# Optimization experiments

Measured on AMD Instinct MI355X. Metric: run time of the kernel, lower is better.

Reference implementation:

```python
import jax, jax.numpy as jnp
import numpy as np

B, D, H = 16384, 64, 128
L = D - 1  # number of per-dimension sub-networks (layers 1..dim-1)
W_SCALE = 0.05  # keep alpha outputs small so exp(alpha) stays well-conditioned


def setup_inputs() -> dict:
    key = jax.random.key(0)
    ks = jax.random.split(key, 8)
    return {
        "x": jax.random.normal(ks[0], (B, D), dtype=jnp.float32),
        "W1": jax.random.normal(ks[1], (L, D - 1, H), dtype=jnp.float32) * W_SCALE,
        "b1": jax.random.normal(ks[2], (L, H), dtype=jnp.float32) * W_SCALE,
        "W2": jax.random.normal(ks[3], (L, H, H), dtype=jnp.float32) * W_SCALE,
        "b2": jax.random.normal(ks[4], (L, H), dtype=jnp.float32) * W_SCALE,
        "W3": jax.random.normal(ks[5], (L, H, 2), dtype=jnp.float32) * W_SCALE,
        "b3": jax.random.normal(ks[6], (L, 2), dtype=jnp.float32) * W_SCALE,
        "initial_param": jax.random.uniform(
            ks[7], (2,), dtype=jnp.float32,
            minval=-np.sqrt(0.5), maxval=np.sqrt(0.5)),
    }


def reference(x, W1, b1, W2, b2, W3, b3, initial_param):
    # x: [B, D]. Layer l (l=0..L-1) corresponds to dim i=l+1 and consumes
    # x[:, :l+1]; we realize the ragged inputs via a triangular mask on W1.
    b, d = x.shape
    # mask[l, j] = 1 if input feature j is visible to layer l (j <= l)
    mask = (jnp.arange(d - 1)[None, :] <= jnp.arange(L)[:, None]).astype(x.dtype)
    W1m = W1 * mask[:, :, None]                       # [L, D-1, H]
    h = jnp.tanh(jnp.einsum('bd,ldh->blh', x[:, :d - 1], W1m) + b1)  # [B, L, H]
    h = jnp.tanh(jnp.einsum('blh,lhk->blk', h, W2) + b2)             # [B, L, H]
    out = jnp.einsum('blh,lho->blo', h, W3) + b3                     # [B, L, 2]
    mu0 = jnp.broadcast_to(initial_param[0], (b, 1))
    a0 = jnp.broadcast_to(initial_param[1], (b, 1))
    mu = jnp.concatenate([mu0, out[..., 0]], axis=1)   # [B, D]
    alpha = jnp.concatenate([a0, out[..., 1]], axis=1)  # [B, D]
    z = (x - mu) * jnp.exp(-alpha)
    log_det = -jnp.sum(alpha, axis=1)                  # [B]
    return z[:, ::-1], log_det
```

## Files before the change

### kernel.cpp

```cpp
#include <hip/hip_runtime.h>
#include <hip/hip_bf16.h>
#include <stdint.h>

#define B_N   16384
#define L_N   63
#define K2LOG2E 2.8853900817779268f
#define LOG2E   1.4426950408889634f

typedef unsigned int   u32;
typedef unsigned short u16;
typedef __attribute__((ext_vector_type(8))) __bf16 bf16x8;
typedef __attribute__((ext_vector_type(4))) float  f32x4;

__device__ __forceinline__ u16 f2b(float f){
  u32 u = __builtin_bit_cast(u32, f);
  u += 0x7fffu + ((u >> 16) & 1u);
  return (u16)(u >> 16);
}
__device__ __forceinline__ u32 pk_bf16(float lo, float hi){
  u32 r;
  asm("v_cvt_pk_bf16_f32 %0, %1, %2" : "=v"(r) : "v"(lo), "v"(hi));
  return r;
}
__device__ __forceinline__ float tanh_sc(float acc){
  float t = __builtin_amdgcn_exp2f(acc);
  float r = __builtin_amdgcn_rcpf(t + 1.0f);
  return fmaf(-2.0f, r, 1.0f);
}

__global__ void k_conv_w1(const float* __restrict__ W1, const float* __restrict__ b1,
                          u16* __restrict__ out){
  __shared__ u16 t[128*64];
  const int l = blockIdx.x, tid = threadIdx.x;
  #pragma unroll
  for (int i = 0; i < 32; ++i) t[i*256 + tid] = 0;
  __syncthreads();
  for (int i = 0; i < 32; ++i){
    int idx = i*256 + tid;
    if (idx < 63*128){
      int d = idx >> 7, n = idx & 127;
      if (d <= l) t[n*64 + d] = f2b(W1[(l*63 + d)*128 + n] * K2LOG2E);
    }
  }
  if (tid < 128) t[tid*64 + 63] = f2b(b1[l*128 + tid] * K2LOG2E);
  __syncthreads();
  uint4* o = (uint4*)(out + l*(128*64));
  const uint4* s4 = (const uint4*)t;
  #pragma unroll
  for (int i = 0; i < 4; ++i) o[i*256 + tid] = s4[i*256 + tid];
}

__global__ void k_conv_w2(const float* __restrict__ W2, const float* __restrict__ b2,
                          u16* __restrict__ out){
  __shared__ u16 t[128*160];
  const int l = blockIdx.x, tid = threadIdx.x;
  #pragma unroll
  for (int i = 0; i < 80; ++i) t[i*256 + tid] = 0;
  __syncthreads();
  #pragma unroll
  for (int i = 0; i < 64; ++i){
    int idx = i*256 + tid;
    int h = idx >> 7, n = idx & 127;
    t[n*160 + h] = f2b(W2[l*16384 + idx] * K2LOG2E);
  }
  if (tid < 128) t[tid*160 + 128] = f2b(b2[l*128 + tid] * K2LOG2E);
  __syncthreads();
  uint4* o = (uint4*)(out + l*(128*160));
  const uint4* s4 = (const uint4*)t;
  #pragma unroll
  for (int i = 0; i < 10; ++i) o[i*256 + tid] = s4[i*256 + tid];
}

__global__ void k_conv_x(const float* __restrict__ x, u16* __restrict__ out){
  int idx = blockIdx.x*256 + threadIdx.x;
  float4 v = ((const float4*)x)[idx];
  ushort4 r;
  r.x = f2b(v.x); r.y = f2b(v.y); r.z = f2b(v.z);
  r.w = ((idx & 15) == 15) ? (u16)0x3F80 : f2b(v.w);
  ((ushort4*)out)[idx] = r;
}

__global__ __launch_bounds__(256, 4)
void k_main(const u16* __restrict__ W1T, const u16* __restrict__ W2T,
            const u16* __restrict__ xbf, const float* __restrict__ x,
            const float* __restrict__ W3, const float* __restrict__ b3,
            float* __restrict__ out, float* __restrict__ alph)
{
  __shared__ __align__(16) char h1b[2*16384];
  __shared__ float2 sc[4][2][64];
  const int tid = threadIdx.x;
  const int ly = blockIdx.y;
  const int bx = blockIdx.x;
  const int wv = tid >> 6;
  const int ln = tid & 63;
  const int c  = ln & 15;
  const int g  = ln >> 4;
  const bool hasB = (ly + 32 < L_N);
  const int rowbase = bx*64;
  const int sx = (c & 7) << 4;

  bf16x8 xf[4][2];
  #pragma unroll
  for (int bt = 0; bt < 4; ++bt)
    #pragma unroll
    for (int s = 0; s < 2; ++s)
      xf[bt][s] = *(const bf16x8*)(xbf + (size_t)(rowbase + bt*16 + c)*64 + s*32 + g*8);

  #pragma unroll
  for (int li = 0; li < 2; ++li){
    if (li == 0 || hasB){
      const int l = ly + li*32;
      const u16* w1p = W1T + l*(128*64);
      char* const hb = h1b + li*16384;
      bf16x8 a0[2], a1[2];
      #pragma unroll
      for (int m = 0; m < 2; ++m){
        const u16* ap = w1p + ((2*wv+m)*16 + c)*64 + g*8;
        a0[m] = *(const bf16x8*)(ap);
        a1[m] = *(const bf16x8*)(ap + 32);
      }
      f32x4 acc[2][4] = {};
      #pragma unroll
      for (int m = 0; m < 2; ++m)
        #pragma unroll
        for (int bt = 0; bt < 4; ++bt){
          acc[m][bt] = __builtin_amdgcn_mfma_f32_16x16x32_bf16(a0[m], xf[bt][0], acc[m][bt], 0,0,0);
          acc[m][bt] = __builtin_amdgcn_mfma_f32_16x16x32_bf16(a1[m], xf[bt][1], acc[m][bt], 0,0,0);
        }
      #pragma unroll
      for (int m = 0; m < 2; ++m){
        int h0 = (2*wv+m)*16 + g*4;
        #pragma unroll
        for (int bt = 0; bt < 4; ++bt){
          u32 p0 = pk_bf16(tanh_sc(acc[m][bt][0]), tanh_sc(acc[m][bt][1]));
          u32 p1 = pk_bf16(tanh_sc(acc[m][bt][2]), tanh_sc(acc[m][bt][3]));
          int b = bt*16 + c;
          *(uint2*)(hb + b*256 + ((h0*2) ^ sx)) = make_uint2(p0, p1);
        }
      }
    }
  }
  __syncthreads();

  uint4 cw; cw.x = (g == 0) ? 0x00003F80u : 0u; cw.y = cw.z = cw.w = 0u;
  const bf16x8 cf = __builtin_bit_cast(bf16x8, cw);

  float part[2][4][2] = {};
  #pragma unroll
  for (int li = 0; li < 2; ++li){
    if (li == 0 || hasB){
      const int l = ly + li*32;
      const u16* w2p = W2T + l*(128*160);
      const char* const hb = h1b + li*16384;
      f32x4 acc2[2][4] = {};
      #pragma unroll
      for (int s = 0; s < 4; ++s){
        bf16x8 a0 = *(const bf16x8*)(w2p + ((2*wv+0)*16 + c)*160 + s*32 + g*8);
        bf16x8 a1 = *(const bf16x8*)(w2p + ((2*wv+1)*16 + c)*160 + s*32 + g*8);
        #pragma unroll
        for (int bt = 0; bt < 4; ++bt){
          int b = bt*16 + c;
          bf16x8 hf = *(const bf16x8*)(hb + b*256 + ((s*64 + g*16) ^ sx));
          acc2[0][bt] = __builtin_amdgcn_mfma_f32_16x16x32_bf16(a0, hf, acc2[0][bt], 0,0,0);
          acc2[1][bt] = __builtin_amdgcn_mfma_f32_16x16x32_bf16(a1, hf, acc2[1][bt], 0,0,0);
        }
      }
      {
        bf16x8 ab0 = *(const bf16x8*)(w2p + ((2*wv+0)*16 + c)*160 + 128 + g*8);
        bf16x8 ab1 = *(const bf16x8*)(w2p + ((2*wv+1)*16 + c)*160 + 128 + g*8);
        #pragma unroll
        for (int bt = 0; bt < 4; ++bt){
          acc2[0][bt] = __builtin_amdgcn_mfma_f32_16x16x32_bf16(ab0, cf, acc2[0][bt], 0,0,0);
          acc2[1][bt] = __builtin_amdgcn_mfma_f32_16x16x32_bf16(ab1, cf, acc2[1][bt], 0,0,0);
        }
      }
      #pragma unroll
      for (int m = 0; m < 2; ++m){
        int q = (2*wv+m)*4 + g;
        float4 w3a = ((const float4*)(W3 + l*256))[q*2 + 0];
        float4 w3b = ((const float4*)(W3 + l*256))[q*2 + 1];
        float w30[4] = { w3a.x, w3a.z, w3b.x, w3b.z };
        float w31[4] = { w3a.y, w3a.w, w3b.y, w3b.w };
        #pragma unroll
        for (int bt = 0; bt < 4; ++bt)
          #pragma unroll
          for (int r = 0; r < 4; ++r){
            float h2 = tanh_sc(acc2[m][bt][r]);
            part[li][bt][0] = fmaf(h2, w30[r], part[li][bt][0]);
            part[li][bt][1] = fmaf(h2, w31[r], part[li][bt][1]);
          }
      }
    }
  }

  #pragma unroll
  for (int li = 0; li < 2; ++li)
    #pragma unroll
    for (int bt = 0; bt < 4; ++bt)
      #pragma unroll
      for (int o = 0; o < 2; ++o){
        float v = part[li][bt][o];
        v += __shfl_xor(v, 16, 64);
        v += __shfl_xor(v, 32, 64);
        part[li][bt][o] = v;
      }
  if (g == 0){
    #pragma unroll
    for (int li = 0; li < 2; ++li)
      #pragma unroll
      for (int bt = 0; bt < 4; ++bt)
        sc[wv][li][bt*16 + c] = make_float2(part[li][bt][0], part[li][bt][1]);
  }
  __syncthreads();

  if (tid < 128){
    int li = tid >> 6, r = tid & 63;
    if (li == 0 || hasB){
      int l = ly + li*32;
      int row = rowbase + r;
      float2 s0 = sc[0][li][r], s1 = sc[1][li][r], s2 = sc[2][li][r], s3 = sc[3][li][r];
      float muv = s0.x + s1.x + s2.x + s3.x + b3[l*2 + 0];
      float alv = s0.y + s1.y + s2.y + s3.y + b3[l*2 + 1];
      float xv  = x[(size_t)row*64 + l + 1];
      out[(size_t)row*64 + 62 - l] = (xv - muv) * __builtin_amdgcn_exp2f(-alv * LOG2E);
      alph[(size_t)row*64 + l + 1] = alv;
    }
  }
}

__global__ void k_fin(const float* __restrict__ x, const float* __restrict__ alph,
                      const float* __restrict__ ip, float* __restrict__ out)
{
  int row = blockIdx.x*4 + (threadIdx.x >> 6);
  int d   = threadIdx.x & 63;
  float a = (d == 0) ? ip[1] : alph[(size_t)row*64 + d];
  float s = a;
  #pragma unroll
  for (int off = 32; off; off >>= 1) s += __shfl_xor(s, off, 64);
  if (d == 0){
    out[(size_t)row*64 + 63] = (x[(size_t)row*64] - ip[0]) * __builtin_amdgcn_exp2f(-a * LOG2E);
    out[(size_t)B_N*64 + row] = -s;
  }
}

extern "C" void kernel_launch(void* const* d_in, const int* in_sizes, int n_in,
                              void* d_out, int out_size, void* d_ws, size_t ws_size,
                              hipStream_t stream)
{
  const float* x  = (const float*)d_in[0];
  const float* W1 = (const float*)d_in[1];
  const float* b1 = (const float*)d_in[2];
  const float* W2 = (const float*)d_in[3];
  const float* b2 = (const float*)d_in[4];
  const float* W3 = (const float*)d_in[5];
  const float* b3 = (const float*)d_in[6];
  const float* ip = (const float*)d_in[7];

  char* ws = (char*)d_ws;
  u16*   w1t  = (u16*)(ws);
  u16*   w2t  = (u16*)(ws + 1048576);
  u16*   xbf  = (u16*)(ws + 3670016);
  float* alph = (float*)(ws + 5767168);
  if (ws_size < 9961472) return;

  k_conv_w1<<<L_N, 256, 0, stream>>>(W1, b1, w1t);
  k_conv_w2<<<L_N, 256, 0, stream>>>(W2, b2, w2t);
  k_conv_x<<<(B_N*64/4)/256, 256, 0, stream>>>(x, xbf);

  dim3 grid(B_N/64, 32);
  k_main<<<grid, 256, 0, stream>>>(w1t, w2t, xbf, x, W3, b3,
                                   (float*)d_out, alph);

  k_fin<<<B_N/4, 256, 0, stream>>>(x, alph, ip, (float*)d_out);
}
```

Measured before the change: 148.5 us.

## Merge prep kernels and split main kernel across eight waves per block

The three conversion kernels (W1, W2, x to bf16) become one launch, with extra blocks handling x, which removes two kernel launches. The main kernel moves from 256 to 512 threads, so each wave owns one 16-column hidden tile instead of two. This halves per-wave accumulator registers and raises occupancy, with the cross-wave reduction widened to eight partials. x fragments are now loaded inside the layer loop instead of being preloaded, and s_setprio is raised around the MFMA section.

```diff
diff --git a/kernel.cpp b/kernel.cpp
--- a/kernel.cpp
+++ b/kernel.cpp
@@ -28,10 +28,23 @@
   return fmaf(-2.0f, r, 1.0f);
 }
 
-__global__ void k_conv_w1(const float* __restrict__ W1, const float* __restrict__ b1,
-                          u16* __restrict__ out){
-  __shared__ u16 t[128*64];
-  const int l = blockIdx.x, tid = threadIdx.x;
+__global__ void k_prep(const float* __restrict__ W1, const float* __restrict__ b1,
+                       const float* __restrict__ W2, const float* __restrict__ b2,
+                       const float* __restrict__ x,
+                       u16* __restrict__ w1t, u16* __restrict__ w2t,
+                       u16* __restrict__ xbf){
+  const int bid = blockIdx.x, tid = threadIdx.x;
+  if (bid >= L_N){
+    int idx = (bid - L_N)*256 + tid;
+    float4 v = ((const float4*)x)[idx];
+    ushort4 r;
+    r.x = f2b(v.x); r.y = f2b(v.y); r.z = f2b(v.z);
+    r.w = ((idx & 15) == 15) ? (u16)0x3F80 : f2b(v.w);
+    ((ushort4*)xbf)[idx] = r;
+    return;
+  }
+  __shared__ u16 t[128*160];
+  const int l = bid;
   #pragma unroll
   for (int i = 0; i < 32; ++i) t[i*256 + tid] = 0;
   __syncthreads();
@@ -44,16 +57,13 @@
   }
   if (tid < 128) t[tid*64 + 63] = f2b(b1[l*128 + tid] * K2LOG2E);
   __syncthreads();
-  uint4* o = (uint4*)(out + l*(128*64));
-  const uint4* s4 = (const uint4*)t;
-  #pragma unroll
-  for (int i = 0; i < 4; ++i) o[i*256 + tid] = s4[i*256 + tid];
-}
-
-__global__ void k_conv_w2(const float* __restrict__ W2, const float* __restrict__ b2,
-                          u16* __restrict__ out){
-  __shared__ u16 t[128*160];
-  const int l = blockIdx.x, tid = threadIdx.x;
+  {
+    uint4* o = (uint4*)(w1t + l*(128*64));
+    const uint4* s4 = (const uint4*)t;
+    #pragma unroll
+    for (int i = 0; i < 4; ++i) o[i*256 + tid] = s4[i*256 + tid];
+  }
+  __syncthreads();
   #pragma unroll
   for (int i = 0; i < 80; ++i) t[i*256 + tid] = 0;
   __syncthreads();
@@ -65,29 +75,22 @@
   }
   if (tid < 128) t[tid*160 + 128] = f2b(b2[l*128 + tid] * K2LOG2E);
   __syncthreads();
-  uint4* o = (uint4*)(out + l*(128*160));
-  const uint4* s4 = (const uint4*)t;
-  #pragma unroll
-  for (int i = 0; i < 10; ++i) o[i*256 + tid] = s4[i*256 + tid];
-}
-
-__global__ void k_conv_x(const float* __restrict__ x, u16* __restrict__ out){
-  int idx = blockIdx.x*256 + threadIdx.x;
-  float4 v = ((const float4*)x)[idx];
-  ushort4 r;
-  r.x = f2b(v.x); r.y = f2b(v.y); r.z = f2b(v.z);
-  r.w = ((idx & 15) == 15) ? (u16)0x3F80 : f2b(v.w);
-  ((ushort4*)out)[idx] = r;
-}
-
-__global__ __launch_bounds__(256, 4)
+  {
+    uint4* o = (uint4*)(w2t + l*(128*160));
+    const uint4* s4 = (const uint4*)t;
+    #pragma unroll
+    for (int i = 0; i < 10; ++i) o[i*256 + tid] = s4[i*256 + tid];
+  }
+}
+
+__global__ __launch_bounds__(512, 8)
 void k_main(const u16* __restrict__ W1T, const u16* __restrict__ W2T,
             const u16* __restrict__ xbf, const float* __restrict__ x,
             const float* __restrict__ W3, const float* __restrict__ b3,
             float* __restrict__ out, float* __restrict__ alph)
 {
   __shared__ __align__(16) char h1b[2*16384];
-  __shared__ float2 sc[4][2][64];
+  __shared__ float2 sc[8][2][64];
   const int tid = threadIdx.x;
   const int ly = blockIdx.y;
   const int bx = blockIdx.x;
@@ -99,44 +102,30 @@
   const int rowbase = bx*64;
   const int sx = (c & 7) << 4;
 
-  bf16x8 xf[4][2];
-  #pragma unroll
-  for (int bt = 0; bt < 4; ++bt)
-    #pragma unroll
-    for (int s = 0; s < 2; ++s)
-      xf[bt][s] = *(const bf16x8*)(xbf + (size_t)(rowbase + bt*16 + c)*64 + s*32 + g*8);
-
   #pragma unroll
   for (int li = 0; li < 2; ++li){
     if (li == 0 || hasB){
       const int l = ly + li*32;
-      const u16* w1p = W1T + l*(128*64);
+      const u16* w1p = W1T + l*(128*64) + (wv*16 + c)*64 + g*8;
+      bf16x8 a0 = *(const bf16x8*)(w1p);
+      bf16x8 a1 = *(const bf16x8*)(w1p + 32);
       char* const hb = h1b + li*16384;
-      bf16x8 a0[2], a1[2];
-      #pragma unroll
-      for (int m = 0; m < 2; ++m){
-        const u16* ap = w1p + ((2*wv+m)*16 + c)*64 + g*8;
-        a0[m] = *(const bf16x8*)(ap);
-        a1[m] = *(const bf16x8*)(ap + 32);
-      }
-      f32x4 acc[2][4] = {};
-      #pragma unroll
-      for (int m = 0; m < 2; ++m)
-        #pragma unroll
-        for (int bt = 0; bt < 4; ++bt){
-          acc[m][bt] = __builtin_amdgcn_mfma_f32_16x16x32_bf16(a0[m], xf[bt][0], acc[m][bt], 0,0,0);
-          acc[m][bt] = __builtin_amdgcn_mfma_f32_16x16x32_bf16(a1[m], xf[bt][1], acc[m][bt], 0,0,0);
-        }
-      #pragma unroll
-      for (int m = 0; m < 2; ++m){
-        int h0 = (2*wv+m)*16 + g*4;
-        #pragma unroll
-        for (int bt = 0; bt < 4; ++bt){
-          u32 p0 = pk_bf16(tanh_sc(acc[m][bt][0]), tanh_sc(acc[m][bt][1]));
-          u32 p1 = pk_bf16(tanh_sc(acc[m][bt][2]), tanh_sc(acc[m][bt][3]));
-          int b = bt*16 + c;
-          *(uint2*)(hb + b*256 + ((h0*2) ^ sx)) = make_uint2(p0, p1);
-        }
+      f32x4 acc[4] = {};
+      #pragma unroll
+      for (int bt = 0; bt < 4; ++bt){
+        const u16* xr = xbf + (size_t)(rowbase + bt*16 + c)*64 + g*8;
+        bf16x8 x0 = *(const bf16x8*)(xr);
+        bf16x8 x1 = *(const bf16x8*)(xr + 32);
+        acc[bt] = __builtin_amdgcn_mfma_f32_16x16x32_bf16(a0, x0, acc[bt], 0,0,0);
+        acc[bt] = __builtin_amdgcn_mfma_f32_16x16x32_bf16(a1, x1, acc[bt], 0,0,0);
+      }
+      const int h0 = wv*16 + g*4;
+      #pragma unroll
+      for (int bt = 0; bt < 4; ++bt){
+        u32 p0 = pk_bf16(tanh_sc(acc[bt][0]), tanh_sc(acc[bt][1]));
+        u32 p1 = pk_bf16(tanh_sc(acc[bt][2]), tanh_sc(acc[bt][3]));
+        int b = bt*16 + c;
+        *(uint2*)(hb + b*256 + ((h0*2) ^ sx)) = make_uint2(p0, p1);
       }
     }
   }
@@ -150,60 +139,52 @@
   for (int li = 0; li < 2; ++li){
     if (li == 0 || hasB){
       const int l = ly + li*32;
-      const u16* w2p = W2T + l*(128*160);
+      const u16* w2p = W2T + l*(128*160) + (wv*16 + c)*160 + g*8;
       const char* const hb = h1b + li*16384;
-      f32x4 acc2[2][4] = {};
+      f32x4 acc2[4] = {};
+      __builtin_amdgcn_s_setprio(1);
       #pragma unroll
       for (int s = 0; s < 4; ++s){
-        bf16x8 a0 = *(const bf16x8*)(w2p + ((2*wv+0)*16 + c)*160 + s*32 + g*8);
-        bf16x8 a1 = *(const bf16x8*)(w2p + ((2*wv+1)*16 + c)*160 + s*32 + g*8);
+        bf16x8 a = *(const bf16x8*)(w2p + s*32);
         #pragma unroll
         for (int bt = 0; bt < 4; ++bt){
           int b = bt*16 + c;
           bf16x8 hf = *(const bf16x8*)(hb + b*256 + ((s*64 + g*16) ^ sx));
-          acc2[0][bt] = __builtin_amdgcn_mfma_f32_16x16x32_bf16(a0, hf, acc2[0][bt], 0,0,0);
-          acc2[1][bt] = __builtin_amdgcn_mfma_f32_16x16x32_bf16(a1, hf, acc2[1][bt], 0,0,0);
+          acc2[bt] = __builtin_amdgcn_mfma_f32_16x16x32_bf16(a, hf, acc2[bt], 0,0,0);
         }
       }
       {
-        bf16x8 ab0 = *(const bf16x8*)(w2p + ((2*wv+0)*16 + c)*160 + 128 + g*8);
-        bf16x8 ab1 = *(const bf16x8*)(w2p + ((2*wv+1)*16 + c)*160 + 128 + g*8);
-        #pragma unroll
-        for (int bt = 0; bt < 4; ++bt){
-          acc2[0][bt] = __builtin_amdgcn_mfma_f32_16x16x32_bf16(ab0, cf, acc2[0][bt], 0,0,0);
-          acc2[1][bt] = __builtin_amdgcn_mfma_f32_16x16x32_bf16(ab1, cf, acc2[1][bt], 0,0,0);
-        }
-      }
-      #pragma unroll
-      for (int m = 0; m < 2; ++m){
-        int q = (2*wv+m)*4 + g;
-        float4 w3a = ((const float4*)(W3 + l*256))[q*2 + 0];
-        float4 w3b = ((const float4*)(W3 + l*256))[q*2 + 1];
-        float w30[4] = { w3a.x, w3a.z, w3b.x, w3b.z };
-        float w31[4] = { w3a.y, w3a.w, w3b.y, w3b.w };
+        bf16x8 ab = *(const bf16x8*)(w2p + 128);
         #pragma unroll
         for (int bt = 0; bt < 4; ++bt)
-          #pragma unroll
-          for (int r = 0; r < 4; ++r){
-            float h2 = tanh_sc(acc2[m][bt][r]);
-            part[li][bt][0] = fmaf(h2, w30[r], part[li][bt][0]);
-            part[li][bt][1] = fmaf(h2, w31[r], part[li][bt][1]);
-          }
-      }
+          acc2[bt] = __builtin_amdgcn_mfma_f32_16x16x32_bf16(ab, cf, acc2[bt], 0,0,0);
+      }
+      __builtin_amdgcn_s_setprio(0);
+      int q = wv*4 + g;
+      float4 w3a = ((const float4*)(W3 + l*256))[q*2 + 0];
+      float4 w3b = ((const float4*)(W3 + l*256))[q*2 + 1];
+      float w30[4] = { w3a.x, w3a.z, w3b.x, w3b.z };
+      float w31[4] = { w3a.y, w3a.w, w3b.y, w3b.w };
+      #pragma unroll
+      for (int bt = 0; bt < 4; ++bt)
+        #pragma unroll
+        for (int r = 0; r < 4; ++r){
+          float h2 = tanh_sc(acc2[bt][r]);
+          part[li][bt][0] = fmaf(h2, w30[r], part[li][bt][0]);
+          part[li][bt][1] = fmaf(h2, w31[r], part[li][bt][1]);
+        }
     }
   }
 
   #pragma unroll
   for (int li = 0; li < 2; ++li)
     #pragma unroll
-    for (int bt = 0; bt < 4; ++bt)
-      #pragma unroll
-      for (int o = 0; o < 2; ++o){
-        float v = part[li][bt][o];
-        v += __shfl_xor(v, 16, 64);
-        v += __shfl_xor(v, 32, 64);
-        part[li][bt][o] = v;
-      }
+    for (int bt = 0; bt < 4; ++bt){
+      float v0 = part[li][bt][0], v1 = part[li][bt][1];
+      v0 += __shfl_xor(v0, 16, 64); v0 += __shfl_xor(v0, 32, 64);
+      v1 += __shfl_xor(v1, 16, 64); v1 += __shfl_xor(v1, 32, 64);
+      part[li][bt][0] = v0; part[li][bt][1] = v1;
+    }
   if (g == 0){
     #pragma unroll
     for (int li = 0; li < 2; ++li)
@@ -218,10 +199,13 @@
     if (li == 0 || hasB){
       int l = ly + li*32;
       int row = rowbase + r;
-      float2 s0 = sc[0][li][r], s1 = sc[1][li][r], s2 = sc[2][li][r], s3 = sc[3][li][r];
-      float muv = s0.x + s1.x + s2.x + s3.x + b3[l*2 + 0];
-      float alv = s0.y + s1.y + s2.y + s3.y + b3[l*2 + 1];
-      float xv  = x[(size_t)row*64 + l + 1];
+      float muv = b3[l*2 + 0], alv = b3[l*2 + 1];
+      #pragma unroll
+      for (int w = 0; w < 8; ++w){
+        float2 s = sc[w][li][r];
+        muv += s.x; alv += s.y;
+      }
+      float xv = x[(size_t)row*64 + l + 1];
       out[(size_t)row*64 + 62 - l] = (xv - muv) * __builtin_amdgcn_exp2f(-alv * LOG2E);
       alph[(size_t)row*64 + l + 1] = alv;
     }
@@ -263,12 +247,11 @@
   float* alph = (float*)(ws + 5767168);
   if (ws_size < 9961472) return;
 
-  k_conv_w1<<<L_N, 256, 0, stream>>>(W1, b1, w1t);
-  k_conv_w2<<<L_N, 256, 0, stream>>>(W2, b2, w2t);
-  k_conv_x<<<(B_N*64/4)/256, 256, 0, stream>>>(x, xbf);
+  k_prep<<<L_N + (B_N*64/4)/256, 256, 0, stream>>>(W1, b1, W2, b2, x,
+                                                   w1t, w2t, xbf);
 
   dim3 grid(B_N/64, 32);
-  k_main<<<grid, 256, 0, stream>>>(w1t, w2t, xbf, x, W3, b3,
+  k_main<<<grid, 512, 0, stream>>>(w1t, w2t, xbf, x, W3, b3,
                                    (float*)d_out, alph);
 
   k_fin<<<B_N/4, 256, 0, stream>>>(x, alph, ip, (float*)d_out);
```

After: 224.8 us. +51.4%, slower.
